# Performance work log

Measured on AMD Instinct MI355X. Metric: run time of the kernel, lower is better.

## Reference

```python
import jax, jax.numpy as jnp
import numpy as np

B, N, D, H = 4, 2048, 768, 12
HD = D // H
SCALE = HD ** -0.5


def setup_inputs() -> dict:
    key = jax.random.key(0)
    k1, k2, k3 = jax.random.split(key, 3)
    x = jax.random.normal(k1, (B, N, D), dtype=jnp.float32)
    w_qkv = jax.random.normal(k2, (D, 3 * D), dtype=jnp.float32) * (D ** -0.5)
    w_proj = jax.random.normal(k3, (D, D), dtype=jnp.float32) * (D ** -0.5)
    b_proj = jnp.zeros((D,), dtype=jnp.float32)
    return {"x": x, "w_qkv": w_qkv, "w_proj": w_proj, "b_proj": b_proj}


def reference(x, w_qkv, w_proj, b_proj):
    b, n, d = x.shape
    qkv = x @ w_qkv                      # [b, n, 3d]
    q, k, v = jnp.split(qkv, 3, axis=-1)
    # [b, n, d] -> [b, h, n, hd]
    split_heads = lambda t: t.reshape(b, n, H, HD).transpose(0, 2, 1, 3)
    q, k, v = split_heads(q), split_heads(k), split_heads(v)
    dots = jnp.einsum('bhqd,bhkd->bhqk', q, k) * SCALE   # [b, h, n, n]
    attn = jax.nn.softmax(dots, axis=-1)
    q_attn = attn[:, :, 0, :]            # attention row of query token 0: [b, h, n]
    # dropout p=0 (eval) -> identity
    out = jnp.einsum('bhqk,bhkd->bhqd', attn, v)          # [b, h, n, hd]
    out = out.transpose(0, 2, 1, 3).reshape(b, n, d)      # [b, n, d]
    return out @ w_proj + b_proj, q_attn
```

## Files before the change

### kernel.cpp

```cpp
#include <hip/hip_runtime.h>


typedef unsigned short u16;
typedef __attribute__((ext_vector_type(8))) short bf8;
typedef __attribute__((ext_vector_type(4))) short bf4;
typedef __attribute__((ext_vector_type(4))) float f4;

#define MFMA16(a, b, c) __builtin_amdgcn_mfma_f32_16x16x32_bf16((a), (b), (c), 0, 0, 0)

#if __has_builtin(__builtin_amdgcn_exp2f)
#define EXP2(x) __builtin_amdgcn_exp2f(x)
#else
#define EXP2(x) __expf((x) * 0.6931471805599453f)
#endif

__device__ __forceinline__ float b2f(u16 h) {
  union { unsigned u; float f; } v; v.u = ((unsigned)h) << 16; return v.f;
}
__device__ __forceinline__ u16 f2b(float f) {
  union { float f; unsigned u; } v; v.f = f;
  unsigned r = v.u + 0x7fffu + ((v.u >> 16) & 1u);
  return (u16)(r >> 16);
}
__device__ __forceinline__ u16 f2bt(float f) {
  union { float f; unsigned u; } v; v.f = f;
  return (u16)(v.u >> 16);
}

__global__ __launch_bounds__(256) void detect_dtype(
    const u16* __restrict__ x, unsigned* __restrict__ flag) {
  __shared__ int any;
  if (threadIdx.x == 0) any = 0;
  __syncthreads();
  unsigned b = x[2 * threadIdx.x];
  unsigned e = (b >> 7) & 0xFF;
  if (e >= 0x8E) atomicOr(&any, 1);
  __syncthreads();
  if (threadIdx.x == 0) *flag = (unsigned)(any ? 1 : 0);
}

__global__ __launch_bounds__(256) void convert_bf16(
    const void* __restrict__ in, u16* __restrict__ out, int n,
    const unsigned* __restrict__ flag) {
  const int f32 = (int)*flag;
  for (int i = blockIdx.x * 256 + threadIdx.x; i < n; i += gridDim.x * 256)
    out[i] = f32 ? f2b(((const float*)in)[i]) : ((const u16*)in)[i];
}

__global__ __launch_bounds__(256) void transpose_any(
    const void* __restrict__ in, u16* __restrict__ out, int R, int C,
    const unsigned* __restrict__ flag) {
  __shared__ u16 tile[32][33];
  const int f32 = (int)*flag;
  const int bx = blockIdx.x * 32;
  const int by = blockIdx.y * 32;
  const int tx = threadIdx.x & 31, ty = threadIdx.x >> 5;
#pragma unroll
  for (int i = 0; i < 4; i++) {
    size_t idx = (size_t)(by + ty + i * 8) * C + bx + tx;
    tile[ty + i * 8][tx] = f32 ? f2b(((const float*)in)[idx]) : ((const u16*)in)[idx];
  }
  __syncthreads();
#pragma unroll
  for (int i = 0; i < 4; i++)
    out[(size_t)(bx + ty + i * 8) * R + by + tx] = tile[tx][ty + i * 8];
}

__global__ __launch_bounds__(256) void transpose_v(
    const u16* __restrict__ qkv, u16* __restrict__ Vt) {
  __shared__ u16 tile[64][65];
  const int n0 = blockIdx.x * 64, h = blockIdx.y, b = blockIdx.z;
  {
    const int d = threadIdx.x & 63, nq = threadIdx.x >> 6;
#pragma unroll
    for (int i = 0; i < 16; i++) {
      int n = i * 4 + nq;
      tile[n][d] = qkv[(size_t)(b * 2048 + n0 + n) * 2304 + 1536 + h * 64 + d];
    }
  }
  __syncthreads();
  {
    const int n = threadIdx.x & 63, dq = threadIdx.x >> 6;
    const int n2 = (n & ~31) | (((n >> 2) & 3) << 3) | (((n >> 4) & 1) << 2) | (n & 3);
#pragma unroll
    for (int i = 0; i < 16; i++) {
      int d2 = i * 4 + dq;
      Vt[(size_t)((b * 12 + h) * 64 + d2) * 2048 + n0 + n2] = tile[n][d2];
    }
  }
}

template <int BIAS>
__global__ __launch_bounds__(256) void gemm_bt(
    const u16* __restrict__ A, const u16* __restrict__ Bt,
    const void* __restrict__ bias, void* __restrict__ C,
    int M, int Ncols, int K, const unsigned* __restrict__ outflag) {
  const int STR = 56;
  __shared__ alignas(16) u16 Al[128 * 56];
  __shared__ alignas(16) u16 Bl[128 * 56];
  const int t = threadIdx.x;
  const int lane = t & 63, wave = t >> 6;
  const int wr = wave >> 1, wc = wave & 1;
  const int quad = lane >> 4, l16 = lane & 15;
  const int bm = blockIdx.y * 128, bn = blockIdx.x * 128;
  const int f32o = outflag ? (int)*outflag : 0;
  f4 acc[4][4] = {};
  for (int k0 = 0; k0 < K; k0 += 32) {
    __syncthreads();
#pragma unroll
    for (int i = 0; i < 2; i++) {
      int s = i * 256 + t;
      int row = s >> 2, c8 = (s & 3) * 8;
      *(bf8*)&Al[row * STR + c8] = *(const bf8*)(A + (size_t)(bm + row) * K + k0 + c8);
      *(bf8*)&Bl[row * STR + c8] = *(const bf8*)(Bt + (size_t)(bn + row) * K + k0 + c8);
    }
    __syncthreads();
    bf8 af[4], bfr[4];
#pragma unroll
    for (int mt = 0; mt < 4; mt++)
      af[mt] = *(const bf8*)&Al[(wr * 64 + mt * 16 + l16) * STR + quad * 8];
#pragma unroll
    for (int nt = 0; nt < 4; nt++)
      bfr[nt] = *(const bf8*)&Bl[(wc * 64 + nt * 16 + l16) * STR + quad * 8];
#pragma unroll
    for (int mt = 0; mt < 4; mt++)
#pragma unroll
      for (int nt = 0; nt < 4; nt++)
        acc[mt][nt] = MFMA16(af[mt], bfr[nt], acc[mt][nt]);
  }
#pragma unroll
  for (int mt = 0; mt < 4; mt++) {
    int row = bm + wr * 64 + mt * 16 + quad * 4;
#pragma unroll
    for (int nt = 0; nt < 4; nt++) {
      int col = bn + wc * 64 + nt * 16 + l16;
      float bv = 0.f;
      if (BIAS)
        bv = f32o ? ((const float*)bias)[col] : b2f(((const u16*)bias)[col]);
#pragma unroll
      for (int r = 0; r < 4; r++) {
        size_t idx = (size_t)(row + r) * Ncols + col;
        float v = acc[mt][nt][r] + bv;
        if (f32o) ((float*)C)[idx] = v; else ((u16*)C)[idx] = f2b(v);
      }
    }
  }
}

__global__ __launch_bounds__(256, 3) void flash_attn(
    const u16* __restrict__ qkv, const u16* __restrict__ Vt,
    u16* __restrict__ O) {
  const int STR = 72;
  __shared__ alignas(16) u16 Kl[64 * 72];
  __shared__ alignas(16) u16 Vl[64 * 72];
  const int t = threadIdx.x, lane = t & 63, wave = t >> 6;
  const int quad = lane >> 4, l16 = lane & 15;
  const int id = blockIdx.x;
  const int bh = (id & 7) + 8 * (id >> 7);
  const int qtile = (id >> 3) & 15;
  const int b = bh / 12, h = bh - b * 12;
  const int q0 = qtile * 128 + wave * 32;
  const float SCALE2 = 0.125f * 1.44269504089f;
  const float M0 = 16.f;
  bf8 qf[2][2];
#pragma unroll
  for (int qt = 0; qt < 2; qt++) {
    const u16* Qr = qkv + (size_t)(b * 2048 + q0 + qt * 16 + l16) * 2304 + h * 64;
    bf8 r0 = *(const bf8*)(Qr + quad * 8);
    bf8 r1 = *(const bf8*)(Qr + 32 + quad * 8);
#pragma unroll
    for (int j = 0; j < 8; j++) {
      qf[qt][0][j] = (short)f2b(b2f((u16)r0[j]) * SCALE2);
      qf[qt][1][j] = (short)f2b(b2f((u16)r1[j]) * SCALE2);
    }
  }
  const u16* Kb = qkv + (size_t)(b * 2048) * 2304 + 768 + h * 64;
  const u16* Vb = Vt + (size_t)((b * 12 + h) * 64) * 2048;
  const int srow = t >> 3, sc8 = (t & 7) * 8;
  const int srow2 = srow + 32;
  f4 o[2][4] = {};
  float lpart[2] = {0.f, 0.f};

  bf8 kreg0 = *(const bf8*)(Kb + (size_t)srow * 2304 + sc8);
  bf8 kreg1 = *(const bf8*)(Kb + (size_t)srow2 * 2304 + sc8);
  bf8 vreg0 = *(const bf8*)(Vb + (size_t)srow * 2048 + sc8);
  bf8 vreg1 = *(const bf8*)(Vb + (size_t)srow2 * 2048 + sc8);

  for (int i = 0; i < 32; i++) {
    __syncthreads();
    *(bf8*)&Kl[srow * STR + sc8] = kreg0;
    *(bf8*)&Kl[srow2 * STR + sc8] = kreg1;
    *(bf8*)&Vl[srow * STR + sc8] = vreg0;
    *(bf8*)&Vl[srow2 * STR + sc8] = vreg1;
    __syncthreads();
    if (i < 31) {
      const u16* Kn = Kb + (size_t)(i * 64 + 64) * 2304;
      const u16* Vn = Vb + (i * 64 + 64);
      kreg0 = *(const bf8*)(Kn + (size_t)srow * 2304 + sc8);
      kreg1 = *(const bf8*)(Kn + (size_t)srow2 * 2304 + sc8);
      vreg0 = *(const bf8*)(Vn + (size_t)srow * 2048 + sc8);
      vreg1 = *(const bf8*)(Vn + (size_t)srow2 * 2048 + sc8);
    }
    bf8 pf[2][2];
#pragma unroll
    for (int kt = 0; kt < 4; kt++) {
      bf8 kf0 = *(const bf8*)&Kl[(kt * 16 + l16) * STR + quad * 8];
      bf8 kf1 = *(const bf8*)&Kl[(kt * 16 + l16) * STR + 32 + quad * 8];
#pragma unroll
      for (int qt = 0; qt < 2; qt++) {
        f4 z = {};
        z = MFMA16(kf0, qf[qt][0], z);
        z = MFMA16(kf1, qf[qt][1], z);
        float e0 = EXP2(z[0] - M0);
        float e1 = EXP2(z[1] - M0);
        float e2 = EXP2(z[2] - M0);
        float e3 = EXP2(z[3] - M0);
        lpart[qt] += (e0 + e1) + (e2 + e3);
        pf[qt][kt >> 1][(kt & 1) * 4 + 0] = (short)f2bt(e0);
        pf[qt][kt >> 1][(kt & 1) * 4 + 1] = (short)f2bt(e1);
        pf[qt][kt >> 1][(kt & 1) * 4 + 2] = (short)f2bt(e2);
        pf[qt][kt >> 1][(kt & 1) * 4 + 3] = (short)f2bt(e3);
      }
    }
#pragma unroll
    for (int pair = 0; pair < 2; pair++) {
#pragma unroll
      for (int nt = 0; nt < 4; nt++) {
        bf8 vf = *(const bf8*)&Vl[(nt * 16 + l16) * STR + pair * 32 + quad * 8];
        o[0][nt] = MFMA16(vf, pf[0][pair], o[0][nt]);
        o[1][nt] = MFMA16(vf, pf[1][pair], o[1][nt]);
      }
    }
  }
#pragma unroll
  for (int qt = 0; qt < 2; qt++) {
    float l = lpart[qt];
    l += __shfl_xor(l, 16, 64);
    l += __shfl_xor(l, 32, 64);
    float inv = 1.f / l;
    size_t row = (size_t)(b * 2048 + q0 + qt * 16 + l16) * 768 + h * 64;
#pragma unroll
    for (int nt = 0; nt < 4; nt++) {
      bf4 pk = {(short)f2b(o[qt][nt][0] * inv), (short)f2b(o[qt][nt][1] * inv),
                (short)f2b(o[qt][nt][2] * inv), (short)f2b(o[qt][nt][3] * inv)};
      *(bf4*)&O[row + nt * 16 + quad * 4] = pk;
    }
  }
}

__global__ __launch_bounds__(256) void qattn_row0(
    const u16* __restrict__ qkv, void* __restrict__ out,
    const unsigned* __restrict__ flag) {
  const int bh = blockIdx.x, b = bh / 12, h = bh % 12;
  __shared__ float qs[64];
  __shared__ float sv[2048];
  __shared__ float red[8];
  const int t = threadIdx.x;
  const int f32o = (int)*flag;
  if (t < 64) qs[t] = b2f(qkv[(size_t)(b * 2048) * 2304 + h * 64 + t]);
  __syncthreads();
  float lmax = -1e30f;
  for (int k = t; k < 2048; k += 256) {
    const u16* Kr = qkv + (size_t)(b * 2048 + k) * 2304 + 768 + h * 64;
    float acc = 0.f;
#pragma unroll
    for (int j = 0; j < 8; j++) {
      bf8 kv = *(const bf8*)(Kr + j * 8);
#pragma unroll
      for (int d = 0; d < 8; d++) acc += qs[j * 8 + d] * b2f((u16)kv[d]);
    }
    acc *= 0.125f;
    sv[k] = acc;
    lmax = fmaxf(lmax, acc);
  }
#pragma unroll
  for (int off = 32; off >= 1; off >>= 1) lmax = fmaxf(lmax, __shfl_xor(lmax, off, 64));
  if ((t & 63) == 0) red[t >> 6] = lmax;
  __syncthreads();
  const float bmax = fmaxf(fmaxf(red[0], red[1]), fmaxf(red[2], red[3]));
  float lsum = 0.f;
  for (int k = t; k < 2048; k += 256) {
    float e = __expf(sv[k] - bmax);
    sv[k] = e;
    lsum += e;
  }
#pragma unroll
  for (int off = 32; off >= 1; off >>= 1) lsum += __shfl_xor(lsum, off, 64);
  if ((t & 63) == 0) red[4 + (t >> 6)] = lsum;
  __syncthreads();
  const float inv = 1.f / (red[4] + red[5] + red[6] + red[7]);
  for (int k = t; k < 2048; k += 256) {
    size_t idx = (size_t)6291456 + (size_t)bh * 2048 + k;
    float v = sv[k] * inv;
    if (f32o) ((float*)out)[idx] = v; else ((u16*)out)[idx] = f2b(v);
  }
}

extern "C" void kernel_launch(void* const* d_in, const int* in_sizes, int n_in,
                              void* d_out, int out_size, void* d_ws, size_t ws_size,
                              hipStream_t stream) {
  const void* x_raw      = d_in[0];
  const void* w_qkv_raw  = d_in[1];
  const void* w_proj_raw = d_in[2];
  const void* b_proj_raw = d_in[3];
  char* ws = (char*)d_ws;
  unsigned* flag = (unsigned*)ws;
  u16* xbf    = (u16*)(ws + 256);
  u16* wqkvT  = (u16*)(ws + 12583168);
  u16* wprojT = (u16*)(ws + 16122112);
  u16* qkv    = (u16*)(ws + 17301760);
  u16* Vt     = (u16*)(ws + 55050496);
  u16* attn   = xbf;

  detect_dtype<<<1, 256, 0, stream>>>((const u16*)x_raw, flag);
  convert_bf16<<<2048, 256, 0, stream>>>(x_raw, xbf, 6291456, flag);
  transpose_any<<<dim3(2304 / 32, 768 / 32), 256, 0, stream>>>(w_qkv_raw, wqkvT, 768, 2304, flag);
  transpose_any<<<dim3(768 / 32, 768 / 32), 256, 0, stream>>>(w_proj_raw, wprojT, 768, 768, flag);
  gemm_bt<0><<<dim3(2304 / 128, 8192 / 128), 256, 0, stream>>>(
      xbf, wqkvT, nullptr, qkv, 8192, 2304, 768, nullptr);
  transpose_v<<<dim3(2048 / 64, 12, 4), 256, 0, stream>>>(qkv, Vt);
  flash_attn<<<dim3(768), 256, 0, stream>>>(qkv, Vt, attn);
  qattn_row0<<<dim3(48), 256, 0, stream>>>(qkv, d_out, flag);
  gemm_bt<1><<<dim3(768 / 128, 8192 / 128), 256, 0, stream>>>(
      attn, wprojT, b_proj_raw, d_out, 8192, 768, 768, flag);
}
```

Before: 255.5 us.

## Use direct global-to-LDS loads in GEMM and reuse flash-attn probabilities for row 0

The GEMM tile loads now go straight from global memory into LDS with global_load_lds, replacing the register round-trip. The unpadded 32-wide LDS rows may cause bank conflicts on the MFMA fragment reads. The flash attention kernel now also writes the unnormalized exp scores and row sum for query 0 of each head when the workspace is large enough. A small normalization kernel then uses them in place of the separate qattn_row0 kernel, which recomputed the QK dot products and softmax. The fused path depends on ws_size and adds a conditional store inside the attention inner loop.

```diff
diff --git a/kernel.cpp b/kernel.cpp
--- a/kernel.cpp
+++ b/kernel.cpp
@@ -25,6 +25,11 @@
 __device__ __forceinline__ u16 f2bt(float f) {
   union { float f; unsigned u; } v; v.f = f;
   return (u16)(v.u >> 16);
+}
+__device__ __forceinline__ void gload16(const u16* g, u16* l) {
+  __builtin_amdgcn_global_load_lds(
+      (const __attribute__((address_space(1))) void*)g,
+      (__attribute__((address_space(3))) void*)l, 16, 0, 0);
 }
 
 __global__ __launch_bounds__(256) void detect_dtype(
@@ -95,33 +100,33 @@
     const u16* __restrict__ A, const u16* __restrict__ Bt,
     const void* __restrict__ bias, void* __restrict__ C,
     int M, int Ncols, int K, const unsigned* __restrict__ outflag) {
-  const int STR = 56;
-  __shared__ alignas(16) u16 Al[128 * 56];
-  __shared__ alignas(16) u16 Bl[128 * 56];
+  __shared__ alignas(16) u16 Al[128 * 32];
+  __shared__ alignas(16) u16 Bl[128 * 32];
   const int t = threadIdx.x;
   const int lane = t & 63, wave = t >> 6;
   const int wr = wave >> 1, wc = wave & 1;
   const int quad = lane >> 4, l16 = lane & 15;
   const int bm = blockIdx.y * 128, bn = blockIdx.x * 128;
   const int f32o = outflag ? (int)*outflag : 0;
+  const int grow = lane >> 2, gcol = (lane & 3) * 8;
   f4 acc[4][4] = {};
   for (int k0 = 0; k0 < K; k0 += 32) {
     __syncthreads();
 #pragma unroll
-    for (int i = 0; i < 2; i++) {
-      int s = i * 256 + t;
-      int row = s >> 2, c8 = (s & 3) * 8;
-      *(bf8*)&Al[row * STR + c8] = *(const bf8*)(A + (size_t)(bm + row) * K + k0 + c8);
-      *(bf8*)&Bl[row * STR + c8] = *(const bf8*)(Bt + (size_t)(bn + row) * K + k0 + c8);
+    for (int c = 0; c < 2; c++) {
+      int chunk = wave * 2 + c;
+      int row = chunk * 16 + grow;
+      gload16(A + (size_t)(bm + row) * K + k0 + gcol, &Al[chunk * 512]);
+      gload16(Bt + (size_t)(bn + row) * K + k0 + gcol, &Bl[chunk * 512]);
     }
     __syncthreads();
     bf8 af[4], bfr[4];
 #pragma unroll
     for (int mt = 0; mt < 4; mt++)
-      af[mt] = *(const bf8*)&Al[(wr * 64 + mt * 16 + l16) * STR + quad * 8];
+      af[mt] = *(const bf8*)&Al[(wr * 64 + mt * 16 + l16) * 32 + quad * 8];
 #pragma unroll
     for (int nt = 0; nt < 4; nt++)
-      bfr[nt] = *(const bf8*)&Bl[(wc * 64 + nt * 16 + l16) * STR + quad * 8];
+      bfr[nt] = *(const bf8*)&Bl[(wc * 64 + nt * 16 + l16) * 32 + quad * 8];
 #pragma unroll
     for (int mt = 0; mt < 4; mt++)
 #pragma unroll
@@ -149,7 +154,7 @@
 
 __global__ __launch_bounds__(256, 3) void flash_attn(
     const u16* __restrict__ qkv, const u16* __restrict__ Vt,
-    u16* __restrict__ O) {
+    u16* __restrict__ O, float* __restrict__ qe, float* __restrict__ lout) {
   const int STR = 72;
   __shared__ alignas(16) u16 Kl[64 * 72];
   __shared__ alignas(16) u16 Vl[64 * 72];
@@ -160,6 +165,7 @@
   const int qtile = (id >> 3) & 15;
   const int b = bh / 12, h = bh - b * 12;
   const int q0 = qtile * 128 + wave * 32;
+  const bool dumpP = (qe != nullptr) && (qtile == 0) && (wave == 0);
   const float SCALE2 = 0.125f * 1.44269504089f;
   const float M0 = 16.f;
   bf8 qf[2][2];
@@ -216,6 +222,10 @@
         float e2 = EXP2(z[2] - M0);
         float e3 = EXP2(z[3] - M0);
         lpart[qt] += (e0 + e1) + (e2 + e3);
+        if (qt == 0 && dumpP && l16 == 0) {
+          f4 ev = {e0, e1, e2, e3};
+          *(f4*)&qe[bh * 2048 + i * 64 + kt * 16 + quad * 4] = ev;
+        }
         pf[qt][kt >> 1][(kt & 1) * 4 + 0] = (short)f2bt(e0);
         pf[qt][kt >> 1][(kt & 1) * 4 + 1] = (short)f2bt(e1);
         pf[qt][kt >> 1][(kt & 1) * 4 + 2] = (short)f2bt(e2);
@@ -237,6 +247,7 @@
     float l = lpart[qt];
     l += __shfl_xor(l, 16, 64);
     l += __shfl_xor(l, 32, 64);
+    if (qt == 0 && dumpP && lane == 0) lout[bh] = l;
     float inv = 1.f / l;
     size_t row = (size_t)(b * 2048 + q0 + qt * 16 + l16) * 768 + h * 64;
 #pragma unroll
@@ -245,6 +256,19 @@
                 (short)f2b(o[qt][nt][2] * inv), (short)f2b(o[qt][nt][3] * inv)};
       *(bf4*)&O[row + nt * 16 + quad * 4] = pk;
     }
+  }
+}
+
+__global__ __launch_bounds__(256) void qattn_norm(
+    const float* __restrict__ qe, const float* __restrict__ lout,
+    void* __restrict__ out, const unsigned* __restrict__ flag) {
+  const int bh = blockIdx.x;
+  const int f32o = (int)*flag;
+  const float inv = 1.f / lout[bh];
+  for (int k = threadIdx.x; k < 2048; k += 256) {
+    size_t idx = (size_t)6291456 + (size_t)bh * 2048 + k;
+    float v = qe[bh * 2048 + k] * inv;
+    if (f32o) ((float*)out)[idx] = v; else ((u16*)out)[idx] = f2b(v);
   }
 }
 
@@ -310,7 +334,10 @@
   u16* wprojT = (u16*)(ws + 16122112);
   u16* qkv    = (u16*)(ws + 17301760);
   u16* Vt     = (u16*)(ws + 55050496);
+  float* qe   = (float*)(ws + 67633408);
+  float* lout = (float*)(ws + 68026624);
   u16* attn   = xbf;
+  const bool fused = ws_size >= 68026816ull;
 
   detect_dtype<<<1, 256, 0, stream>>>((const u16*)x_raw, flag);
   convert_bf16<<<2048, 256, 0, stream>>>(x_raw, xbf, 6291456, flag);
@@ -319,8 +346,13 @@
   gemm_bt<0><<<dim3(2304 / 128, 8192 / 128), 256, 0, stream>>>(
       xbf, wqkvT, nullptr, qkv, 8192, 2304, 768, nullptr);
   transpose_v<<<dim3(2048 / 64, 12, 4), 256, 0, stream>>>(qkv, Vt);
-  flash_attn<<<dim3(768), 256, 0, stream>>>(qkv, Vt, attn);
-  qattn_row0<<<dim3(48), 256, 0, stream>>>(qkv, d_out, flag);
+  flash_attn<<<dim3(768), 256, 0, stream>>>(qkv, Vt, attn,
+                                            fused ? qe : nullptr,
+                                            fused ? lout : nullptr);
+  if (fused)
+    qattn_norm<<<dim3(48), 256, 0, stream>>>(qe, lout, d_out, flag);
+  else
+    qattn_row0<<<dim3(48), 256, 0, stream>>>(qkv, d_out, flag);
   gemm_bt<1><<<dim3(768 / 128, 8192 / 128), 256, 0, stream>>>(
       attn, wprojT, b_proj_raw, d_out, 8192, 768, 768, flag);
 }
```

Measured after the change: 241.3 us. -5.6%, faster.
